# Optimization experiments

Hardware: AMD Instinct MI355X
Metric: run time of the kernel (lower is better)

Reference implementation:

```python
import jax, jax.numpy as jnp
import numpy as np
import math

NUM_HEADS = 8
LN_EPS = 1e-5


def layer_norm(x, g, b):
    mu = x.mean(-1, keepdims=True)
    var = ((x - mu) ** 2).mean(-1, keepdims=True)
    return (x - mu) * jax.lax.rsqrt(var + LN_EPS) * g + b


def typed_linear(x, W, types):
    # x: [E, in], W: [R, in, out], types: [E] int -> [E, out]
    out = jnp.zeros((x.shape[0], W.shape[-1]), x.dtype)
    for r in range(W.shape[0]):  # small fixed relation count
        out = out + jnp.where((types == r)[:, None], x @ W[r], 0.0)
    return out


def setup_inputs() -> dict:
    key = jax.random.key(0)
    ks = jax.random.split(key, 20)
    N, M, E = 50000, 10000, 100000
    in_dim, e_dim, out_dim, td = 128, 32, 128, 32
    R, T = 8, 4
    inp = {
        'src_h': jax.random.normal(ks[0], (N, in_dim), jnp.float32),
        'src_tw': jax.random.normal(ks[1], (N, td), jnp.float32),
        'src_tb': jax.random.normal(ks[2], (N, td), jnp.float32),
        'edge_h': jax.random.normal(ks[3], (E, e_dim), jnp.float32),
        'date': jax.random.uniform(ks[4], (E,), jnp.float32),
        'src_idx': jax.random.randint(ks[5], (E,), 0, N, jnp.int32),
        'dst_idx': jax.random.randint(ks[6], (E,), 0, M, jnp.int32),
        'etype': jax.random.randint(ks[7], (E,), 0, R, jnp.int32),
        'ntype': jax.random.randint(ks[8], (M,), 0, T, jnp.int32),
    }
    def w(k, shape):
        return jax.random.normal(k, shape, jnp.float32) / math.sqrt(shape[-2])
    inp['Wq'] = w(ks[9], (R, in_dim, out_dim))
    inp['Wk'] = w(ks[10], (R, in_dim + e_dim, out_dim))
    inp['Wv'] = w(ks[11], (R, in_dim + e_dim, out_dim))
    inp['Wa'] = w(ks[12], (T, out_dim, out_dim))
    inp['h_bias'] = jnp.zeros((T, out_dim), jnp.float32)
    inp['skip'] = jnp.ones((T,), jnp.float32)
    inp['src_ln_g'] = jnp.ones((in_dim + e_dim,), jnp.float32)
    inp['src_ln_b'] = jnp.zeros((in_dim + e_dim,), jnp.float32)
    inp['dst_ln_g'] = jnp.ones((in_dim,), jnp.float32)
    inp['dst_ln_b'] = jnp.zeros((in_dim,), jnp.float32)
    return inp


def reference(src_h, src_tw, src_tb, edge_h, date, src_idx, dst_idx, etype, ntype,
              Wq, Wk, Wv, Wa, h_bias, skip, src_ln_g, src_ln_b, dst_ln_g, dst_ln_b):
    M = ntype.shape[0]
    out_dim = Wq.shape[-1]
    H = NUM_HEADS
    hs = out_dim // H
    td = src_tw.shape[-1]
    t = date[:, None]  # [E,1]

    # gather src / dst node data per edge (dst nodes are first M src rows)
    h_s, tw_s, tb_s = src_h[src_idx], src_tw[src_idx], src_tb[src_idx]
    h_d, tw_d, tb_d = src_h[dst_idx], src_tw[dst_idx], src_tb[dst_idx]

    # time2vec modulation of the first td channels
    dia_s = jnp.concatenate([jnp.sin(tw_s * t + tb_s) * h_s[:, :td], h_s[:, td:]], -1)
    dia_d = jnp.concatenate([jnp.sin(tw_d * t + tb_d) * h_d[:, :td], h_d[:, td:]], -1)
    dia_s = jnp.concatenate([dia_s, edge_h], -1)  # [E, in_dim+e_dim]

    # pre_norm
    dia_s = layer_norm(dia_s, src_ln_g, src_ln_b)
    dia_d = layer_norm(dia_d, dst_ln_g, dst_ln_b)

    q = typed_linear(dia_d, Wq, etype).reshape(-1, H, hs)
    k = typed_linear(dia_s, Wk, etype).reshape(-1, H, hs)
    v = typed_linear(dia_s, Wv, etype).reshape(-1, H, hs)

    a = (q * k).sum(-1) / math.sqrt(out_dim)  # [E, H]

    # edge_softmax: segment softmax over destination nodes
    amax = jax.lax.stop_gradient(jax.ops.segment_max(a, dst_idx, num_segments=M))
    ex = jnp.exp(a - amax[dst_idx])
    denom = jax.ops.segment_sum(ex, dst_idx, num_segments=M)
    alpha = ex / denom[dst_idx]  # [E, H]

    # weighted scatter-sum aggregation
    m = (v * alpha[..., None]).reshape(-1, out_dim)  # [E, out_dim]
    h = jax.ops.segment_sum(m, dst_idx, num_segments=M)  # [M, out_dim]

    h = h + h_bias[ntype]
    gate = jax.nn.sigmoid(skip[ntype])[:, None]
    h = typed_linear(h, Wa, ntype)  # dropout is identity at eval
    dst_h = src_h[:M]
    return h * gate + dst_h * (1.0 - gate)
```

## Files before the change

### kernel.cpp

```cpp
#include <hip/hip_runtime.h>


typedef __attribute__((ext_vector_type(8))) short short8;
typedef __attribute__((ext_vector_type(4))) float f32x4;

__device__ __forceinline__ unsigned short f2bf(float f){
  union { float f; unsigned u; } x; x.f = f;
  unsigned r = x.u + 0x7FFFu + ((x.u >> 16) & 1u);
  return (unsigned short)(r >> 16);
}
__device__ __forceinline__ float bf2f(unsigned short b){
  union { unsigned u; float f; } x; x.u = ((unsigned)b) << 16;
  return x.f;
}


__global__ void k_zero(int* __restrict__ p, int n){
  int i = blockIdx.x*256 + threadIdx.x;
  if(i < n) p[i] = 0;
}

__global__ __launch_bounds__(256) void k_hist(
    const int* __restrict__ etype, const int* __restrict__ dst_idx,
    const int* __restrict__ ntype,
    int* cnt_e, int* cnt_d, int* cnt_n, int E, int M){
  __shared__ int le[8], ln[4];
  int tid = threadIdx.x;
  if(tid < 8) le[tid] = 0;
  if(tid < 4) ln[tid] = 0;
  __syncthreads();
  int g = blockIdx.x*256 + tid;
  if(g < E){ atomicAdd(&le[etype[g]], 1); atomicAdd(&cnt_d[dst_idx[g]], 1); }
  if(g < M){ atomicAdd(&ln[ntype[g]], 1); }
  __syncthreads();
  if(tid < 8 && le[tid]) atomicAdd(&cnt_e[tid], le[tid]);
  if(tid < 4 && ln[tid]) atomicAdd(&cnt_n[tid], ln[tid]);
}

__global__ __launch_bounds__(1024) void k_scan(const int* __restrict__ cnt_e, int* off_e,
                                               const int* __restrict__ cnt_n, int* off_n,
                                               const int* __restrict__ cnt_d, int* off_d, int M){
  __shared__ int part[1024];
  int tid = threadIdx.x;
  if(tid == 0){
    int s = 0;
    for(int i=0;i<8;i++){ off_e[i]=s; s+=cnt_e[i]; } off_e[8]=s;
    s = 0;
    for(int i=0;i<4;i++){ off_n[i]=s; s+=cnt_n[i]; } off_n[4]=s;
  }
  int per = (M + 1023) >> 10;
  int s = 0;
  for(int j=0;j<per;j++){ int idx = tid*per + j; if(idx < M) s += cnt_d[idx]; }
  part[tid] = s; __syncthreads();
  for(int o=1;o<1024;o<<=1){
    int v = (tid >= o) ? part[tid-o] : 0;
    __syncthreads();
    part[tid] += v;
    __syncthreads();
  }
  int run = (tid == 0) ? 0 : part[tid-1];
  for(int j=0;j<per;j++){
    int idx = tid*per + j;
    if(idx < M){ off_d[idx] = run; run += cnt_d[idx]; }
  }
  if(tid == 1023) off_d[M] = run;
}

__global__ __launch_bounds__(256) void k_scatter(
    const int* __restrict__ etype, const int* __restrict__ src_idx,
    const int* __restrict__ dst_idx, const float* __restrict__ date,
    const int* __restrict__ ntype,
    const int* __restrict__ off_e, int* cur_e,
    const int* __restrict__ off_d, int* cur_d,
    const int* __restrict__ off_n, int* cur_n,
    int4* __restrict__ recs, int* dstlist, int* nperm, int* npos, int E, int M){
  __shared__ int lcnt[8], lbase[8], lnc[4], lnb[4];
  int tid = threadIdx.x;
  if(tid < 8) lcnt[tid] = 0;
  if(tid < 4) lnc[tid] = 0;
  __syncthreads();
  int g = blockIdx.x*256 + tid;
  int r = 0, lrank = 0, t = 0, nrank = 0;
  bool inE = (g < E), inM = (g < M);
  if(inE){ r = etype[g]; lrank = atomicAdd(&lcnt[r], 1); }
  if(inM){ t = ntype[g]; nrank = atomicAdd(&lnc[t], 1); }
  __syncthreads();
  if(tid < 8 && lcnt[tid]) lbase[tid] = atomicAdd(&cur_e[tid], lcnt[tid]);
  if(tid < 4 && lnc[tid])  lnb[tid]   = atomicAdd(&cur_n[tid], lnc[tid]);
  __syncthreads();
  if(inE){
    int p = off_e[r] + lbase[r] + lrank;
    int4 rec;
    rec.x = src_idx[g]; rec.y = dst_idx[g]; rec.z = g;
    rec.w = __float_as_int(date[g]);
    recs[p] = rec;
    int d = rec.y;
    int q = off_d[d] + atomicAdd(&cur_d[d], 1);
    dstlist[q] = p;
  }
  if(inM){
    int np = off_n[t] + lnb[t] + nrank;
    npos[g] = np;
    nperm[np] = g;
  }
}

__global__ void k_convw(const float* __restrict__ Wq, const float* __restrict__ Wk,
                        const float* __restrict__ Wv, const float* __restrict__ Wa,
                        unsigned short* Wq_t, unsigned short* Wk_t,
                        unsigned short* Wv_t, unsigned short* Wa_t){
  int tid = blockIdx.x*256 + threadIdx.x;
  if(tid < 131072){
    int r = tid >> 14, rem = tid & 16383, i = rem >> 7, o = rem & 127;
    Wq_t[(r<<14) + (o<<7) + i] = f2bf(Wq[tid]);
  } else if(tid < 294912){
    int u = tid - 131072;
    int r = u / 20480, rem = u - r*20480, i = rem >> 7, o = rem & 127;
    Wk_t[r*20480 + o*160 + i] = f2bf(Wk[u]);
  } else if(tid < 458752){
    int u = tid - 294912;
    int r = u / 20480, rem = u - r*20480, i = rem >> 7, o = rem & 127;
    Wv_t[r*20480 + o*160 + i] = f2bf(Wv[u]);
  } else if(tid < 524288){
    int u = tid - 458752;
    int r = u >> 14, rem = u & 16383, i = rem >> 7, o = rem & 127;
    Wa_t[(r<<14) + (o<<7) + i] = f2bf(Wa[u]);
  }
}

__global__ __launch_bounds__(256) void k_prep(
  const float* __restrict__ src_h, const float* __restrict__ src_tw, const float* __restrict__ src_tb,
  const float* __restrict__ edge_h, const int4* __restrict__ recs,
  const float* __restrict__ g_s, const float* __restrict__ b_s,
  const float* __restrict__ g_d, const float* __restrict__ b_d,
  unsigned short* __restrict__ dia_s, unsigned short* __restrict__ dia_d, int E)
{
  int p = blockIdx.x*4 + (threadIdx.x >> 6);
  if(p >= E) return;
  int lane = threadIdx.x & 63;
  int4 rec = recs[p];
  int s = rec.x, d = rec.y, e = rec.z;
  float t = __int_as_float(rec.w);

  {
    float2 h2 = *(const float2*)(src_h + (size_t)s*128 + 2*lane);
    float x0 = h2.x, x1 = h2.y;
    if(lane < 16){
      float2 tw2 = *(const float2*)(src_tw + s*32 + 2*lane);
      float2 tb2 = *(const float2*)(src_tb + s*32 + 2*lane);
      x0 = __sinf(tw2.x*t + tb2.x) * h2.x;
      x1 = __sinf(tw2.y*t + tb2.y) * h2.y;
    }
    float e0 = 0.f, e1 = 0.f;
    if(lane >= 16 && lane < 32){
      float2 eh = *(const float2*)(edge_h + (size_t)e*32 + 2*(lane-16));
      e0 = eh.x; e1 = eh.y;
    }
    float s1 = x0+x1+e0+e1, s2 = x0*x0+x1*x1+e0*e0+e1*e1;
    #pragma unroll
    for(int i=1;i<64;i<<=1){ s1 += __shfl_xor(s1,i); s2 += __shfl_xor(s2,i); }
    float mu = s1*(1.f/160.f);
    float var = s2*(1.f/160.f) - mu*mu;
    float sc = rsqrtf(var + 1e-5f);
    float2 g2 = *(const float2*)(g_s + 2*lane);
    float2 b2 = *(const float2*)(b_s + 2*lane);
    float o0 = (x0-mu)*sc*g2.x + b2.x;
    float o1 = (x1-mu)*sc*g2.y + b2.y;
    ((unsigned*)dia_s)[(size_t)p*80 + lane] = (unsigned)f2bf(o0) | ((unsigned)f2bf(o1)<<16);
    if(lane >= 16 && lane < 32){
      float2 g2e = *(const float2*)(g_s + 128 + 2*(lane-16));
      float2 b2e = *(const float2*)(b_s + 128 + 2*(lane-16));
      float q0 = (e0-mu)*sc*g2e.x + b2e.x;
      float q1 = (e1-mu)*sc*g2e.y + b2e.y;
      ((unsigned*)dia_s)[(size_t)p*80 + 48 + lane] = (unsigned)f2bf(q0) | ((unsigned)f2bf(q1)<<16);
    }
  }
  {
    float2 h2 = *(const float2*)(src_h + (size_t)d*128 + 2*lane);
    float y0 = h2.x, y1 = h2.y;
    if(lane < 16){
      float2 tw2 = *(const float2*)(src_tw + d*32 + 2*lane);
      float2 tb2 = *(const float2*)(src_tb + d*32 + 2*lane);
      y0 = __sinf(tw2.x*t + tb2.x) * h2.x;
      y1 = __sinf(tw2.y*t + tb2.y) * h2.y;
    }
    float s1 = y0+y1, s2 = y0*y0+y1*y1;
    #pragma unroll
    for(int i=1;i<64;i<<=1){ s1 += __shfl_xor(s1,i); s2 += __shfl_xor(s2,i); }
    float mu = s1*(1.f/128.f);
    float var = s2*(1.f/128.f) - mu*mu;
    float sc = rsqrtf(var + 1e-5f);
    float2 g2 = *(const float2*)(g_d + 2*lane);
    float2 b2 = *(const float2*)(b_d + 2*lane);
    float o0 = (y0-mu)*sc*g2.x + b2.x;
    float o1 = (y1-mu)*sc*g2.y + b2.y;
    ((unsigned*)dia_d)[(size_t)p*64 + lane] = (unsigned)f2bf(o0) | ((unsigned)f2bf(o1)<<16);
  }
}

__device__ __forceinline__ void stage(const unsigned short* __restrict__ src, int srcld,
                                      unsigned short* dst, int dstld,
                                      int rows, int c16, int tid, int nv){
  int total = rows * c16;
  for(int idx = tid; idx < total; idx += 256){
    int rr = idx / c16, c = idx - rr*c16;
    int4 v = make_int4(0,0,0,0);
    if(rr < nv) v = *(const int4*)(src + (size_t)rr*srcld + c*8);
    *(int4*)(dst + rr*dstld + c*8) = v;
  }
}

template<int KD>
__device__ __forceinline__ void gemm_lds(
  const unsigned short* A, int lda,
  const unsigned short* W, int ldw,
  f32x4* acc, int tid)
{
  int lane = tid & 63, w = tid >> 6, m = lane & 15, quad = lane >> 4;
  #pragma unroll
  for(int i=0;i<8;i++) acc[i] = (f32x4){0.f,0.f,0.f,0.f};
  #pragma unroll
  for(int k0=0; k0<KD; k0+=32){
    short8 b0 = *(const short8*)(W + (w*32 +      m)*ldw + k0 + quad*8);
    short8 b1 = *(const short8*)(W + (w*32 + 16 + m)*ldw + k0 + quad*8);
    #pragma unroll
    for(int rt=0; rt<4; rt++){
      short8 af = *(const short8*)(A + (rt*16 + m)*lda + k0 + quad*8);
      acc[rt*2+0] = __builtin_amdgcn_mfma_f32_16x16x32_bf16(af, b0, acc[rt*2+0], 0,0,0);
      acc[rt*2+1] = __builtin_amdgcn_mfma_f32_16x16x32_bf16(af, b1, acc[rt*2+1], 0,0,0);
    }
  }
}

__global__ __launch_bounds__(256) void k_qkv(
  const unsigned short* __restrict__ dia_d, const unsigned short* __restrict__ dia_s,
  const unsigned short* __restrict__ Wq_t, const unsigned short* __restrict__ Wk_t,
  const unsigned short* __restrict__ Wv_t,
  const int* __restrict__ cnt_e, const int* __restrict__ off_e,
  float* __restrict__ abuf, unsigned short* __restrict__ vbuf)
{
  __shared__ __align__(16) unsigned short U[64*168];
  __shared__ __align__(16) unsigned short Wb[128*168];
  int bid = blockIdx.x;
  int r = -1, tl0 = 0, accT = 0;
  #pragma unroll
  for(int i=0;i<8;i++){
    int n = cnt_e[i], tt = (n + 63) >> 6;
    if(r < 0 && bid < accT + tt){ r = i; tl0 = bid - accT; }
    accT += tt;
  }
  if(r < 0) return;
  int row0 = off_e[r] + tl0*64;
  int nv = min(64, cnt_e[r] - tl0*64);
  int tid = threadIdx.x;
  int lane = tid & 63, w = tid >> 6, m = lane & 15, quad = lane >> 4;

  f32x4 qa[8], ka[8];
  stage(dia_d + (size_t)row0*128, 128, U, 136, 64, 16, tid, nv);
  stage(Wq_t + r*16384, 128, Wb, 136, 128, 16, tid, 128);
  __syncthreads();
  gemm_lds<128>(U, 136, Wb, 136, qa, tid);
  __syncthreads();
  stage(dia_s + (size_t)row0*160, 160, U, 168, 64, 20, tid, nv);
  stage(Wk_t + r*20480, 160, Wb, 168, 128, 20, tid, 128);
  __syncthreads();
  gemm_lds<160>(U, 168, Wb, 168, ka, tid);

  const float inv = 0.08838834764831845f;
  #pragma unroll
  for(int rt=0; rt<4; rt++)
  #pragma unroll
  for(int ct=0; ct<2; ct++){
    #pragma unroll
    for(int reg=0; reg<4; reg++){
      float s = qa[rt*2+ct][reg] * ka[rt*2+ct][reg];
      s += __shfl_xor(s,1); s += __shfl_xor(s,2); s += __shfl_xor(s,4); s += __shfl_xor(s,8);
      int row = rt*16 + quad*4 + reg;
      if(m == 0 && row < nv) abuf[(size_t)(row0+row)*8 + w*2 + ct] = __expf(s * inv);
    }
  }
  __syncthreads();
  stage(Wv_t + r*20480, 160, Wb, 168, 128, 20, tid, 128);
  __syncthreads();
  gemm_lds<160>(U, 168, Wb, 168, qa, tid);
  #pragma unroll
  for(int rt=0; rt<4; rt++)
  #pragma unroll
  for(int ct=0; ct<2; ct++)
  #pragma unroll
  for(int reg=0; reg<4; reg++){
    int row = rt*16 + quad*4 + reg;
    if(row < nv)
      vbuf[(size_t)(row0+row)*128 + w*32 + ct*16 + m] = f2bf(qa[rt*2+ct][reg]);
  }
}

__global__ __launch_bounds__(64) void k_aggr(
  const float* __restrict__ abuf, const unsigned short* __restrict__ vbuf,
  const int* __restrict__ dstlist, const int* __restrict__ off_d,
  const int* __restrict__ npos, const int* __restrict__ ntype,
  const float* __restrict__ h_bias, unsigned short* __restrict__ hpre)
{
  int d = blockIdx.x, lane = threadIdx.x;
  int o0 = off_d[d], cnt = off_d[d+1] - o0;
  int h = lane >> 3;
  float denp = 0.f;
  for(int i = (lane>>3); i < cnt; i += 8)
    denp += abuf[(size_t)dstlist[o0+i]*8 + (lane & 7)];
  denp += __shfl_xor(denp, 8); denp += __shfl_xor(denp, 16); denp += __shfl_xor(denp, 32);
  float dh = __shfl(denp, h);
  float rd = (dh > 0.f) ? (1.f/dh) : 0.f;
  float a0 = 0.f, a1 = 0.f;
  const unsigned* vb = (const unsigned*)vbuf;
  int i = 0;
  for(; i + 4 <= cnt; i += 4){
    int p0 = dstlist[o0+i], p1 = dstlist[o0+i+1], p2 = dstlist[o0+i+2], p3 = dstlist[o0+i+3];
    float l0 = abuf[(size_t)p0*8 + h], l1 = abuf[(size_t)p1*8 + h];
    float l2 = abuf[(size_t)p2*8 + h], l3 = abuf[(size_t)p3*8 + h];
    unsigned v0 = vb[(size_t)p0*64 + lane], v1 = vb[(size_t)p1*64 + lane];
    unsigned v2 = vb[(size_t)p2*64 + lane], v3 = vb[(size_t)p3*64 + lane];
    a0 += l0*bf2f((unsigned short)(v0&0xffff)) + l1*bf2f((unsigned short)(v1&0xffff))
        + l2*bf2f((unsigned short)(v2&0xffff)) + l3*bf2f((unsigned short)(v3&0xffff));
    a1 += l0*bf2f((unsigned short)(v0>>16)) + l1*bf2f((unsigned short)(v1>>16))
        + l2*bf2f((unsigned short)(v2>>16)) + l3*bf2f((unsigned short)(v3>>16));
  }
  for(; i < cnt; i++){
    int p = dstlist[o0+i];
    float al = abuf[(size_t)p*8 + h];
    unsigned v2 = vb[(size_t)p*64 + lane];
    a0 += al * bf2f((unsigned short)(v2 & 0xffff));
    a1 += al * bf2f((unsigned short)(v2 >> 16));
  }
  a0 *= rd; a1 *= rd;
  int t = ntype[d];
  a0 += h_bias[t*128 + 2*lane];
  a1 += h_bias[t*128 + 2*lane + 1];
  ((unsigned*)hpre)[(size_t)npos[d]*64 + lane] =
      (unsigned)f2bf(a0) | ((unsigned)f2bf(a1) << 16);
}

__global__ __launch_bounds__(256) void k_final(
  const unsigned short* __restrict__ hpre, const unsigned short* __restrict__ Wa_t,
  const int* __restrict__ cnt_n, const int* __restrict__ off_n, const int* __restrict__ nperm,
  const float* __restrict__ skip, const float* __restrict__ src_h, float* __restrict__ out)
{
  __shared__ __align__(16) unsigned short U[64*136];
  __shared__ __align__(16) unsigned short Wb[128*136];
  int bid = blockIdx.x;
  int r = -1, tl0 = 0, accT = 0;
  #pragma unroll
  for(int i=0;i<4;i++){
    int n = cnt_n[i], tt = (n + 63) >> 6;
    if(r < 0 && bid < accT + tt){ r = i; tl0 = bid - accT; }
    accT += tt;
  }
  if(r < 0) return;
  int row0 = off_n[r] + tl0*64;
  int nv = min(64, cnt_n[r] - tl0*64);
  float gate = 1.f / (1.f + __expf(-skip[r]));
  int tid = threadIdx.x;
  int lane = tid & 63, w = tid >> 6, m = lane & 15, quad = lane >> 4;
  stage(hpre + (size_t)row0*128, 128, U, 136, 64, 16, tid, nv);
  stage(Wa_t + r*16384, 128, Wb, 136, 128, 16, tid, 128);
  __syncthreads();
  f32x4 acc[8];
  gemm_lds<128>(U, 136, Wb, 136, acc, tid);
  #pragma unroll
  for(int rt=0; rt<4; rt++)
  #pragma unroll
  for(int ct=0; ct<2; ct++)
  #pragma unroll
  for(int reg=0; reg<4; reg++){
    int row = rt*16 + quad*4 + reg;
    if(row < nv){
      int dd = nperm[row0+row];
      int col = w*32 + ct*16 + m;
      out[(size_t)dd*128 + col] = acc[rt*2+ct][reg]*gate + src_h[(size_t)dd*128 + col]*(1.f - gate);
    }
  }
}

extern "C" void kernel_launch(void* const* d_in, const int* in_sizes, int n_in,
                              void* d_out, int out_size, void* d_ws, size_t ws_size,
                              hipStream_t stream)
{
  const float* src_h  = (const float*)d_in[0];
  const float* src_tw = (const float*)d_in[1];
  const float* src_tb = (const float*)d_in[2];
  const float* edge_h = (const float*)d_in[3];
  const float* date   = (const float*)d_in[4];
  const int*   src_idx= (const int*)d_in[5];
  const int*   dst_idx= (const int*)d_in[6];
  const int*   etype  = (const int*)d_in[7];
  const int*   ntype  = (const int*)d_in[8];
  const float* Wq     = (const float*)d_in[9];
  const float* Wk     = (const float*)d_in[10];
  const float* Wv     = (const float*)d_in[11];
  const float* Wa     = (const float*)d_in[12];
  const float* h_bias = (const float*)d_in[13];
  const float* skip   = (const float*)d_in[14];
  const float* g_s    = (const float*)d_in[15];
  const float* b_s    = (const float*)d_in[16];
  const float* g_d    = (const float*)d_in[17];
  const float* b_d    = (const float*)d_in[18];
  float* out = (float*)d_out;

  const int E = in_sizes[4];
  const int M = in_sizes[8];

  char* base = (char*)d_ws;
  size_t off = 0;
  auto alloc = [&](size_t bytes)->char*{
    off = (off + 255) & ~(size_t)255;
    char* p = base + off; off += bytes; return p;
  };
  int* cnt_e = (int*)alloc((size_t)(24 + 2*M)*4);
  int* cur_e = cnt_e + 8;
  int* cnt_n = cur_e + 8;
  int* cur_n = cnt_n + 4;
  int* cnt_d = cur_n + 4;
  int* cur_d = cnt_d + M;
  const int nzero = 24 + 2*M;
  int* off_e = (int*)alloc(9*4);
  int* off_n = (int*)alloc(5*4);
  int* off_d = (int*)alloc((size_t)(M+1)*4);
  int4* recs   = (int4*)alloc((size_t)E*16);
  int* dstlist = (int*)alloc((size_t)E*4);
  int* nperm   = (int*)alloc((size_t)M*4);
  int* npos    = (int*)alloc((size_t)M*4);
  unsigned short* Wq_t = (unsigned short*)alloc((size_t)8*128*128*2);
  unsigned short* Wk_t = (unsigned short*)alloc((size_t)8*160*128*2);
  unsigned short* Wv_t = (unsigned short*)alloc((size_t)8*160*128*2);
  unsigned short* Wa_t = (unsigned short*)alloc((size_t)4*128*128*2);
  unsigned short* dia_d = (unsigned short*)alloc((size_t)E*128*2);
  unsigned short* dia_s = (unsigned short*)alloc((size_t)E*160*2);
  unsigned short* vbuf  = (unsigned short*)alloc((size_t)E*128*2);
  unsigned short* hpre  = (unsigned short*)alloc((size_t)M*128*2);
  float* abuf = (float*)alloc((size_t)E*8*4);

  k_zero<<<dim3((nzero+255)/256), dim3(256), 0, stream>>>(cnt_e, nzero);
  k_hist<<<dim3((E+255)/256), dim3(256), 0, stream>>>(etype, dst_idx, ntype, cnt_e, cnt_d, cnt_n, E, M);
  k_scan<<<dim3(1), dim3(1024), 0, stream>>>(cnt_e, off_e, cnt_n, off_n, cnt_d, off_d, M);
  k_scatter<<<dim3((E+255)/256), dim3(256), 0, stream>>>(etype, src_idx, dst_idx, date, ntype,
      off_e, cur_e, off_d, cur_d, off_n, cur_n, recs, dstlist, nperm, npos, E, M);
  k_convw<<<dim3(2048), dim3(256), 0, stream>>>(Wq, Wk, Wv, Wa, Wq_t, Wk_t, Wv_t, Wa_t);
  k_prep<<<dim3((E+3)/4), dim3(256), 0, stream>>>(src_h, src_tw, src_tb, edge_h, recs,
      g_s, b_s, g_d, b_d, dia_s, dia_d, E);
  k_qkv<<<dim3(E/64 + 9), dim3(256), 0, stream>>>(dia_d, dia_s, Wq_t, Wk_t, Wv_t,
      cnt_e, off_e, abuf, vbuf);
  k_aggr<<<dim3(M), dim3(64), 0, stream>>>(abuf, vbuf, dstlist, off_d, npos, ntype, h_bias, hpre);
  k_final<<<dim3(M/64 + 5), dim3(256), 0, stream>>>(hpre, Wa_t, cnt_n, off_n, nperm, skip, src_h, out);
}
```

Baseline: 305.0 us.

## Make QKV kernel persistent with cached weights; split prep and tile convw

The QKV kernel becomes persistent: 256 blocks each walk a contiguous range of 64-edge tiles. Each block keeps Wq, Wk and Wv for the current relation in a large dynamic LDS buffer and reloads them only when the relation changes, which removes repeated weight staging and the mid-kernel syncs. The weight conversion kernel now transposes through a shared-memory tile so its reads and writes are coalesced. The prep kernel gives the source and destination layer norms to separate wavefronts to raise parallelism. The ~156KB LDS allocation allows only one block per CU, which cuts latency hiding.

```diff
diff --git a/kernel.cpp b/kernel.cpp
--- a/kernel.cpp
+++ b/kernel.cpp
@@ -105,26 +105,32 @@
   }
 }
 
-__global__ void k_convw(const float* __restrict__ Wq, const float* __restrict__ Wk,
-                        const float* __restrict__ Wv, const float* __restrict__ Wa,
-                        unsigned short* Wq_t, unsigned short* Wk_t,
-                        unsigned short* Wv_t, unsigned short* Wa_t){
-  int tid = blockIdx.x*256 + threadIdx.x;
-  if(tid < 131072){
-    int r = tid >> 14, rem = tid & 16383, i = rem >> 7, o = rem & 127;
-    Wq_t[(r<<14) + (o<<7) + i] = f2bf(Wq[tid]);
-  } else if(tid < 294912){
-    int u = tid - 131072;
-    int r = u / 20480, rem = u - r*20480, i = rem >> 7, o = rem & 127;
-    Wk_t[r*20480 + o*160 + i] = f2bf(Wk[u]);
-  } else if(tid < 458752){
-    int u = tid - 294912;
-    int r = u / 20480, rem = u - r*20480, i = rem >> 7, o = rem & 127;
-    Wv_t[r*20480 + o*160 + i] = f2bf(Wv[u]);
-  } else if(tid < 524288){
-    int u = tid - 458752;
-    int r = u >> 14, rem = u & 16383, i = rem >> 7, o = rem & 127;
-    Wa_t[(r<<14) + (o<<7) + i] = f2bf(Wa[u]);
+__global__ __launch_bounds__(256) void k_convw(
+    const float* __restrict__ Wq, const float* __restrict__ Wk,
+    const float* __restrict__ Wv, const float* __restrict__ Wa,
+    unsigned short* Wq_t, unsigned short* Wk_t,
+    unsigned short* Wv_t, unsigned short* Wa_t)
+{
+  __shared__ float tile[32][33];
+  int b = blockIdx.x;
+  const float* src; unsigned short* dst; int K, rem;
+  if(b < 128){       int r = b >> 4;          rem = b & 15;   src = Wq + r*16384; dst = Wq_t + r*16384; K = 128; }
+  else if(b < 288){  int u = b-128; int r = u/20; rem = u - r*20; src = Wk + r*20480; dst = Wk_t + r*20480; K = 160; }
+  else if(b < 448){  int u = b-288; int r = u/20; rem = u - r*20; src = Wv + r*20480; dst = Wv_t + r*20480; K = 160; }
+  else {             int u = b-448; int r = u >> 4; rem = u & 15; src = Wa + r*16384; dst = Wa_t + r*16384; K = 128; }
+  int nkt = K >> 5;
+  int ki = rem % nkt, oj = rem / nkt;
+  int tx = threadIdx.x & 31, ty = threadIdx.x >> 5;
+  #pragma unroll
+  for(int j=0;j<4;j++){
+    int row = ty + j*8;
+    tile[row][tx] = src[(size_t)(ki*32+row)*128 + oj*32 + tx];
+  }
+  __syncthreads();
+  #pragma unroll
+  for(int j=0;j<4;j++){
+    int a = ty + j*8;
+    dst[(size_t)(oj*32+a)*K + ki*32 + tx] = f2bf(tile[tx][a]);
   }
 }
 
@@ -136,13 +142,15 @@
   unsigned short* __restrict__ dia_s, unsigned short* __restrict__ dia_d, int E)
 {
   int p = blockIdx.x*4 + (threadIdx.x >> 6);
-  if(p >= E) return;
+  bool isS = p < E;
+  int pe = isS ? p : p - E;
+  if(pe >= E) return;
   int lane = threadIdx.x & 63;
-  int4 rec = recs[p];
-  int s = rec.x, d = rec.y, e = rec.z;
+  int4 rec = recs[pe];
   float t = __int_as_float(rec.w);
 
-  {
+  if(isS){
+    int s = rec.x, e = rec.z;
     float2 h2 = *(const float2*)(src_h + (size_t)s*128 + 2*lane);
     float x0 = h2.x, x1 = h2.y;
     if(lane < 16){
@@ -166,16 +174,16 @@
     float2 b2 = *(const float2*)(b_s + 2*lane);
     float o0 = (x0-mu)*sc*g2.x + b2.x;
     float o1 = (x1-mu)*sc*g2.y + b2.y;
-    ((unsigned*)dia_s)[(size_t)p*80 + lane] = (unsigned)f2bf(o0) | ((unsigned)f2bf(o1)<<16);
+    ((unsigned*)dia_s)[(size_t)pe*80 + lane] = (unsigned)f2bf(o0) | ((unsigned)f2bf(o1)<<16);
     if(lane >= 16 && lane < 32){
       float2 g2e = *(const float2*)(g_s + 128 + 2*(lane-16));
       float2 b2e = *(const float2*)(b_s + 128 + 2*(lane-16));
       float q0 = (e0-mu)*sc*g2e.x + b2e.x;
       float q1 = (e1-mu)*sc*g2e.y + b2e.y;
-      ((unsigned*)dia_s)[(size_t)p*80 + 48 + lane] = (unsigned)f2bf(q0) | ((unsigned)f2bf(q1)<<16);
-    }
-  }
-  {
+      ((unsigned*)dia_s)[(size_t)pe*80 + 48 + lane] = (unsigned)f2bf(q0) | ((unsigned)f2bf(q1)<<16);
+    }
+  } else {
+    int d = rec.y;
     float2 h2 = *(const float2*)(src_h + (size_t)d*128 + 2*lane);
     float y0 = h2.x, y1 = h2.y;
     if(lane < 16){
@@ -194,7 +202,7 @@
     float2 b2 = *(const float2*)(b_d + 2*lane);
     float o0 = (y0-mu)*sc*g2.x + b2.x;
     float o1 = (y1-mu)*sc*g2.y + b2.y;
-    ((unsigned*)dia_d)[(size_t)p*64 + lane] = (unsigned)f2bf(o0) | ((unsigned)f2bf(o1)<<16);
+    ((unsigned*)dia_d)[(size_t)pe*64 + lane] = (unsigned)f2bf(o0) | ((unsigned)f2bf(o1)<<16);
   }
 }
 
@@ -232,6 +240,13 @@
   }
 }
 
+#define WQ_OFF 0
+#define WK_OFF 17408
+#define WV_OFF 38912
+#define AD_OFF 60416
+#define AS_OFF 69120
+#define QKV_LDS_BYTES 159744
+
 __global__ __launch_bounds__(256) void k_qkv(
   const unsigned short* __restrict__ dia_d, const unsigned short* __restrict__ dia_s,
   const unsigned short* __restrict__ Wq_t, const unsigned short* __restrict__ Wk_t,
@@ -239,59 +254,70 @@
   const int* __restrict__ cnt_e, const int* __restrict__ off_e,
   float* __restrict__ abuf, unsigned short* __restrict__ vbuf)
 {
-  __shared__ __align__(16) unsigned short U[64*168];
-  __shared__ __align__(16) unsigned short Wb[128*168];
-  int bid = blockIdx.x;
-  int r = -1, tl0 = 0, accT = 0;
-  #pragma unroll
-  for(int i=0;i<8;i++){
-    int n = cnt_e[i], tt = (n + 63) >> 6;
-    if(r < 0 && bid < accT + tt){ r = i; tl0 = bid - accT; }
-    accT += tt;
-  }
-  if(r < 0) return;
-  int row0 = off_e[r] + tl0*64;
-  int nv = min(64, cnt_e[r] - tl0*64);
+  extern __shared__ __align__(16) unsigned short sm[];
+  unsigned short* Wq_l = sm + WQ_OFF;
+  unsigned short* Wk_l = sm + WK_OFF;
+  unsigned short* Wv_l = sm + WV_OFF;
+  unsigned short* Ad   = sm + AD_OFF;
+  unsigned short* As   = sm + AS_OFF;
+
   int tid = threadIdx.x;
   int lane = tid & 63, w = tid >> 6, m = lane & 15, quad = lane >> 4;
-
-  f32x4 qa[8], ka[8];
-  stage(dia_d + (size_t)row0*128, 128, U, 136, 64, 16, tid, nv);
-  stage(Wq_t + r*16384, 128, Wb, 136, 128, 16, tid, 128);
-  __syncthreads();
-  gemm_lds<128>(U, 136, Wb, 136, qa, tid);
-  __syncthreads();
-  stage(dia_s + (size_t)row0*160, 160, U, 168, 64, 20, tid, nv);
-  stage(Wk_t + r*20480, 160, Wb, 168, 128, 20, tid, 128);
-  __syncthreads();
-  gemm_lds<160>(U, 168, Wb, 168, ka, tid);
-
+  int tbase[9]; int T = 0;
+  #pragma unroll
+  for(int i=0;i<8;i++){ tbase[i] = T; T += (cnt_e[i] + 63) >> 6; }
+  tbase[8] = T;
+  int NB = gridDim.x;
+  int t0 = (int)(((long long)blockIdx.x * T) / NB);
+  int t1 = (int)(((long long)(blockIdx.x+1) * T) / NB);
+  int cur_r = -1;
   const float inv = 0.08838834764831845f;
-  #pragma unroll
-  for(int rt=0; rt<4; rt++)
-  #pragma unroll
-  for(int ct=0; ct<2; ct++){
+
+  for(int t = t0; t < t1; t++){
+    int r = 0;
+    #pragma unroll
+    for(int i=1;i<8;i++) if(t >= tbase[i]) r = i;
+    int tl = t - tbase[r];
+    int row0 = off_e[r] + tl*64;
+    int nv = min(64, cnt_e[r] - tl*64);
+
+    __syncthreads();
+    if(r != cur_r){
+      stage(Wq_t + r*16384, 128, Wq_l, 136, 128, 16, tid, 128);
+      stage(Wk_t + r*20480, 160, Wk_l, 168, 128, 20, tid, 128);
+      stage(Wv_t + r*20480, 160, Wv_l, 168, 128, 20, tid, 128);
+      cur_r = r;
+    }
+    stage(dia_d + (size_t)row0*128, 128, Ad, 136, 64, 16, tid, nv);
+    stage(dia_s + (size_t)row0*160, 160, As, 168, 64, 20, tid, nv);
+    __syncthreads();
+
+    f32x4 qa[8], ka[8];
+    gemm_lds<128>(Ad, 136, Wq_l, 136, qa, tid);
+    gemm_lds<160>(As, 168, Wk_l, 168, ka, tid);
+    #pragma unroll
+    for(int rt=0; rt<4; rt++)
+    #pragma unroll
+    for(int ct=0; ct<2; ct++){
+      #pragma unroll
+      for(int reg=0; reg<4; reg++){
+        float s = qa[rt*2+ct][reg] * ka[rt*2+ct][reg];
+        s += __shfl_xor(s,1); s += __shfl_xor(s,2); s += __shfl_xor(s,4); s += __shfl_xor(s,8);
+        int row = rt*16 + quad*4 + reg;
+        if(m == 0 && row < nv) abuf[(size_t)(row0+row)*8 + w*2 + ct] = __expf(s * inv);
+      }
+    }
+    gemm_lds<160>(As, 168, Wv_l, 168, qa, tid);
+    #pragma unroll
+    for(int rt=0; rt<4; rt++)
+    #pragma unroll
+    for(int ct=0; ct<2; ct++)
     #pragma unroll
     for(int reg=0; reg<4; reg++){
-      float s = qa[rt*2+ct][reg] * ka[rt*2+ct][reg];
-      s += __shfl_xor(s,1); s += __shfl_xor(s,2); s += __shfl_xor(s,4); s += __shfl_xor(s,8);
       int row = rt*16 + quad*4 + reg;
-      if(m == 0 && row < nv) abuf[(size_t)(row0+row)*8 + w*2 + ct] = __expf(s * inv);
-    }
-  }
-  __syncthreads();
-  stage(Wv_t + r*20480, 160, Wb, 168, 128, 20, tid, 128);
-  __syncthreads();
-  gemm_lds<160>(U, 168, Wb, 168, qa, tid);
-  #pragma unroll
-  for(int rt=0; rt<4; rt++)
-  #pragma unroll
-  for(int ct=0; ct<2; ct++)
-  #pragma unroll
-  for(int reg=0; reg<4; reg++){
-    int row = rt*16 + quad*4 + reg;
-    if(row < nv)
-      vbuf[(size_t)(row0+row)*128 + w*32 + ct*16 + m] = f2bf(qa[rt*2+ct][reg]);
+      if(row < nv)
+        vbuf[(size_t)(row0+row)*128 + w*32 + ct*16 + m] = f2bf(qa[rt*2+ct][reg]);
+    }
   }
 }
 
@@ -438,15 +464,22 @@
   unsigned short* hpre  = (unsigned short*)alloc((size_t)M*128*2);
   float* abuf = (float*)alloc((size_t)E*8*4);
 
+  static bool attr_set = false;
+  if(!attr_set){
+    (void)hipFuncSetAttribute((const void*)k_qkv,
+        hipFuncAttributeMaxDynamicSharedMemorySize, QKV_LDS_BYTES);
+    attr_set = true;
+  }
+
   k_zero<<<dim3((nzero+255)/256), dim3(256), 0, stream>>>(cnt_e, nzero);
   k_hist<<<dim3((E+255)/256), dim3(256), 0, stream>>>(etype, dst_idx, ntype, cnt_e, cnt_d, cnt_n, E, M);
   k_scan<<<dim3(1), dim3(1024), 0, stream>>>(cnt_e, off_e, cnt_n, off_n, cnt_d, off_d, M);
   k_scatter<<<dim3((E+255)/256), dim3(256), 0, stream>>>(etype, src_idx, dst_idx, date, ntype,
       off_e, cur_e, off_d, cur_d, off_n, cur_n, recs, dstlist, nperm, npos, E, M);
-  k_convw<<<dim3(2048), dim3(256), 0, stream>>>(Wq, Wk, Wv, Wa, Wq_t, Wk_t, Wv_t, Wa_t);
-  k_prep<<<dim3((E+3)/4), dim3(256), 0, stream>>>(src_h, src_tw, src_tb, edge_h, recs,
+  k_convw<<<dim3(512), dim3(256), 0, stream>>>(Wq, Wk, Wv, Wa, Wq_t, Wk_t, Wv_t, Wa_t);
+  k_prep<<<dim3((2*E+3)/4), dim3(256), 0, stream>>>(src_h, src_tw, src_tb, edge_h, recs,
       g_s, b_s, g_d, b_d, dia_s, dia_d, E);
-  k_qkv<<<dim3(E/64 + 9), dim3(256), 0, stream>>>(dia_d, dia_s, Wq_t, Wk_t, Wv_t,
+  k_qkv<<<dim3(256), dim3(256), QKV_LDS_BYTES, stream>>>(dia_d, dia_s, Wq_t, Wk_t, Wv_t,
       cnt_e, off_e, abuf, vbuf);
   k_aggr<<<dim3(M), dim3(64), 0, stream>>>(abuf, vbuf, dstlist, off_d, npos, ntype, h_bias, hpre);
   k_final<<<dim3(M/64 + 5), dim3(256), 0, stream>>>(hpre, Wa_t, cnt_n, off_n, nperm, skip, src_h, out);
```

Result: slower. 318.1 us (+4.3%).
